# Kernel tuning notes

Measured on AMD Instinct MI355X. Metric: run time of the kernel, lower is better.

The kernel has to match this reference:

```python
import jax, jax.numpy as jnp
import numpy as np

B, N, IN_DIM, HID, OUT, HEADS = 2, 1024, 64, 64, 64, 4
PHD1, PHD2 = HID // HEADS, OUT // HEADS
SLOPE = 0.2  # PyG GATv2Conv default negative_slope
EPS = 1e-12  # F.normalize eps


def _gatv2_dense(x, Wl, Wr, att, bias, heads, phd, mask):
    """Dense GATv2 layer over a full adjacency mask.
    x: [B,N,Din]; Wl/Wr: [Din, heads*phd]; att: [heads,phd]; bias: [heads*phd];
    mask: [N,N] bool, mask[i,j]=True means edge j->i exists.
    """
    Bb, Nn, _ = x.shape
    xl = (x @ Wl).reshape(Bb, Nn, heads, phd)  # source features
    xr = (x @ Wr).reshape(Bb, Nn, heads, phd)  # target features
    # s[b,i,j,h,p] = leaky_relu(xr[b,i] + xl[b,j])  (GATv2)
    s = jax.nn.leaky_relu(xr[:, :, None] + xl[:, None, :], SLOPE)
    e = jnp.einsum('bijhp,hp->bijh', s, att)  # [B,Ni,Nj,H]
    e = jnp.where(mask[None, :, :, None], e, -jnp.inf)
    alpha = jax.nn.softmax(e, axis=2)  # softmax over source nodes j
    out = jnp.einsum('bijh,bjhp->bihp', alpha, xl).reshape(Bb, Nn, heads * phd)
    return out + bias


def setup_inputs() -> dict:
    key = jax.random.key(0)
    ks = jax.random.split(key, 10)
    sc = 0.1
    return {
        'x': jax.random.normal(ks[0], (B, N, IN_DIM), jnp.float32),
        'embedding': jax.random.normal(ks[1], (N, HID), jnp.float32),
        'Wl1': jax.random.normal(ks[2], (IN_DIM, HEADS * PHD1), jnp.float32) * sc,
        'Wr1': jax.random.normal(ks[3], (IN_DIM, HEADS * PHD1), jnp.float32) * sc,
        'att1': jax.random.normal(ks[4], (HEADS, PHD1), jnp.float32) * sc,
        'b1': jnp.zeros((HEADS * PHD1,), jnp.float32),
        'Wl2': jax.random.normal(ks[5], (HID, HEADS * PHD2), jnp.float32) * sc,
        'Wr2': jax.random.normal(ks[6], (HID, HEADS * PHD2), jnp.float32) * sc,
        'att2': jax.random.normal(ks[7], (HEADS, PHD2), jnp.float32) * sc,
        'b2': jnp.zeros((HEADS * PHD2,), jnp.float32),
    }


def reference(x, embedding, Wl1, Wr1, att1, b1, Wl2, Wr2, att2, b2):
    # AdaptiveAdjacency: cosine-similarity adjacency; only its nonzero pattern is used.
    norm = jnp.maximum(jnp.linalg.norm(embedding, axis=1, keepdims=True), EPS)
    ne = embedding / norm
    adj = ne @ ne.T  # [N,N]
    # edge set = adj.nonzero(); GATv2Conv(add_self_loops=True) guarantees diagonal
    mask = (adj != 0) | jnp.eye(N, dtype=bool)
    h = jax.nn.relu(_gatv2_dense(x, Wl1, Wr1, att1, b1, HEADS, PHD1, mask))
    # dropout(0.3) in eval mode -> identity
    return _gatv2_dense(h, Wl2, Wr2, att2, b2, HEADS, PHD2, mask)
```

## Files before the change

kernel.cpp:

```cpp
#include <hip/hip_runtime.h>
#include <math.h>

#define NN 1024
#define BB 2
#define D 64
#define NHEAD 4
#define PH 16
#define LOG2E 1.4426950408889634f

template <int CTRL>
__device__ __forceinline__ float dpp_mov(float x) {
    int xi = __builtin_bit_cast(int, x);
    int r = __builtin_amdgcn_update_dpp(0, xi, CTRL, 0xF, 0xF, true);
    return __builtin_bit_cast(float, r);
}

__device__ __forceinline__ float dpp_rowsum16(float t) {
    t += dpp_mov<0x111>(t);
    t += dpp_mov<0x112>(t);
    t += dpp_mov<0x114>(t);
    t += dpp_mov<0x118>(t);
    return t;
}

__device__ __forceinline__ float quad_sum4(float t) {
    t += dpp_mov<0xB1>(t);
    t += dpp_mov<0x4E>(t);
    return t;
}

#define MST 65
__global__ __launch_bounds__(256) void k_mask(const float* __restrict__ emb,
                                              unsigned char* __restrict__ mask) {
    __shared__ float As[64 * MST];
    __shared__ float Bs[64 * MST];
    int tid = threadIdx.x;
    int ib = (blockIdx.x & 15) << 6;
    int jb = (blockIdx.x >> 4) << 6;

    #pragma unroll
    for (int r = 0; r < 4; ++r) {
        int q = tid + (r << 8);
        int row = q >> 4, c4 = (q & 15) << 2;
        float4 a = *(const float4*)&emb[(ib + row) * D + c4];
        float4 b = *(const float4*)&emb[(jb + row) * D + c4];
        As[row * MST + c4 + 0] = a.x; As[row * MST + c4 + 1] = a.y;
        As[row * MST + c4 + 2] = a.z; As[row * MST + c4 + 3] = a.w;
        Bs[row * MST + c4 + 0] = b.x; Bs[row * MST + c4 + 1] = b.y;
        Bs[row * MST + c4 + 2] = b.z; Bs[row * MST + c4 + 3] = b.w;
    }
    __syncthreads();

    int i0 = (tid >> 4) << 2;
    int j0 = (tid & 15) << 2;
    float acc[4][4] = {};
    #pragma unroll 8
    for (int k = 0; k < 64; ++k) {
        float a0 = As[(i0 + 0) * MST + k];
        float a1 = As[(i0 + 1) * MST + k];
        float a2 = As[(i0 + 2) * MST + k];
        float a3 = As[(i0 + 3) * MST + k];
        float b0 = Bs[(j0 + 0) * MST + k];
        float b1 = Bs[(j0 + 1) * MST + k];
        float b2 = Bs[(j0 + 2) * MST + k];
        float b3 = Bs[(j0 + 3) * MST + k];
        acc[0][0] = fmaf(a0, b0, acc[0][0]); acc[0][1] = fmaf(a0, b1, acc[0][1]);
        acc[0][2] = fmaf(a0, b2, acc[0][2]); acc[0][3] = fmaf(a0, b3, acc[0][3]);
        acc[1][0] = fmaf(a1, b0, acc[1][0]); acc[1][1] = fmaf(a1, b1, acc[1][1]);
        acc[1][2] = fmaf(a1, b2, acc[1][2]); acc[1][3] = fmaf(a1, b3, acc[1][3]);
        acc[2][0] = fmaf(a2, b0, acc[2][0]); acc[2][1] = fmaf(a2, b1, acc[2][1]);
        acc[2][2] = fmaf(a2, b2, acc[2][2]); acc[2][3] = fmaf(a2, b3, acc[2][3]);
        acc[3][0] = fmaf(a3, b0, acc[3][0]); acc[3][1] = fmaf(a3, b1, acc[3][1]);
        acc[3][2] = fmaf(a3, b2, acc[3][2]); acc[3][3] = fmaf(a3, b3, acc[3][3]);
    }
    #pragma unroll
    for (int r = 0; r < 4; ++r) {
        int gi = ib + i0 + r;
        uchar4 m;
        m.x = (acc[r][0] != 0.f || gi == jb + j0 + 0) ? 1 : 0;
        m.y = (acc[r][1] != 0.f || gi == jb + j0 + 1) ? 1 : 0;
        m.z = (acc[r][2] != 0.f || gi == jb + j0 + 2) ? 1 : 0;
        m.w = (acc[r][3] != 0.f || gi == jb + j0 + 3) ? 1 : 0;
        *(uchar4*)&mask[gi * NN + jb + j0] = m;
    }
}

__global__ __launch_bounds__(256) void k_gemm2(const float* __restrict__ A,
                                               const float* __restrict__ Wl,
                                               const float* __restrict__ Wr,
                                               const float* __restrict__ att,
                                               float* __restrict__ xl,
                                               float* __restrict__ xr,
                                               float* __restrict__ alE) {
    __shared__ float wl[64 * 64];
    __shared__ float wr[64 * 64];
    int tid = threadIdx.x;
    for (int t = tid; t < 4096; t += 256) { wl[t] = Wl[t]; wr[t] = Wr[t]; }
    __syncthreads();
    int r = blockIdx.x * 4 + (tid >> 6);
    int c = tid & 63;
    float av = att[c];
    const float* arow = A + r * 64;
    float accl = 0.f, accr = 0.f;
    #pragma unroll
    for (int p = 0; p < 64; ++p) {
        float a = arow[p];
        accl = fmaf(a, wl[p * 64 + c], accl);
        accr = fmaf(a, wr[p * 64 + c], accr);
    }
    xl[r * 64 + c] = accl;
    xr[r * 64 + c] = accr;
    float t = dpp_rowsum16(accl * av);
    if ((c & 15) == 15) alE[(r << 2) | (c >> 4)] = 0.6f * LOG2E * t;
}

template <bool RELU>
__global__ __launch_bounds__(256, 2) void k_attn(
    const float* __restrict__ xl, const float* __restrict__ xr,
    const float* __restrict__ att, const float* __restrict__ alE,
    const float* __restrict__ bias, const unsigned char* __restrict__ mask,
    float* __restrict__ out)
{
    __shared__ float Opart[4][4][4][64];
    __shared__ float Lpart[4][4][4][NHEAD];

    int tid = threadIdx.x;
    int wave = tid >> 6, lane = tid & 63;
    int h = lane & 3, jl = lane >> 2;
    int b = blockIdx.x >> 8;
    int i0 = (blockIdx.x & 255) << 2;
    int j0 = (wave << 8) + (jl << 4);

    const float* xlb = xl + (b << 16);

    float at[16], xr0f[16], xr1f[16], xr2f[16], xr3f[16];
    {
        const float* ap = att + (h << 2);
        const float* r0 = xr + (((b << 10) + i0) << 6) + (h << 2);
        const float* r1 = r0 + 64;
        const float* r2 = r0 + 128;
        const float* r3 = r0 + 192;
        #pragma unroll
        for (int q = 0; q < 4; ++q) {
            *(float4*)&at[q << 2]   = *(const float4*)(ap + (q << 4));
            *(float4*)&xr0f[q << 2] = *(const float4*)(r0 + (q << 4));
            *(float4*)&xr1f[q << 2] = *(const float4*)(r1 + (q << 4));
            *(float4*)&xr2f[q << 2] = *(const float4*)(r2 + (q << 4));
            *(float4*)&xr3f[q << 2] = *(const float4*)(r3 + (q << 4));
        }
        #pragma unroll
        for (int p = 0; p < 16; ++p) at[p] *= 0.4f * LOG2E;
    }
    float ar0q[4], ar1q[4], ar2q[4], ar3q[4];
    #pragma unroll
    for (int q = 0; q < 4; ++q) {
        float p0 = 0.f, p1 = 0.f, p2 = 0.f, p3 = 0.f;
        #pragma unroll
        for (int r = 0; r < 4; ++r) {
            float a = at[(q << 2) + r];
            p0 = fmaf(a, xr0f[(q << 2) + r], p0);
            p1 = fmaf(a, xr1f[(q << 2) + r], p1);
            p2 = fmaf(a, xr2f[(q << 2) + r], p2);
            p3 = fmaf(a, xr3f[(q << 2) + r], p3);
        }
        ar0q[q] = 1.5f * quad_sum4(p0);
        ar1q[q] = 1.5f * quad_sum4(p1);
        ar2q[q] = 1.5f * quad_sum4(p2);
        ar3q[q] = 1.5f * quad_sum4(p3);
    }

    unsigned mb0 = 0, mb1 = 0, mb2 = 0, mb3 = 0;
    {
        const unsigned* m0p = (const unsigned*)(mask + (i0 + 0) * NN + j0);
        const unsigned* m1p = (const unsigned*)(mask + (i0 + 1) * NN + j0);
        const unsigned* m2p = (const unsigned*)(mask + (i0 + 2) * NN + j0);
        const unsigned* m3p = (const unsigned*)(mask + (i0 + 3) * NN + j0);
        #pragma unroll
        for (int q = 0; q < 4; ++q) {
            unsigned w0 = m0p[q], w1 = m1p[q], w2 = m2p[q], w3 = m3p[q];
            mb0 |= ((((w0 >> 0) & 1) | ((w0 >> 7) & 2) | ((w0 >> 14) & 4) | ((w0 >> 21) & 8)) << (q << 2));
            mb1 |= ((((w1 >> 0) & 1) | ((w1 >> 7) & 2) | ((w1 >> 14) & 4) | ((w1 >> 21) & 8)) << (q << 2));
            mb2 |= ((((w2 >> 0) & 1) | ((w2 >> 7) & 2) | ((w2 >> 14) & 4) | ((w2 >> 21) & 8)) << (q << 2));
            mb3 |= ((((w3 >> 0) & 1) | ((w3 >> 7) & 2) | ((w3 >> 14) & 4) | ((w3 >> 21) & 8)) << (q << 2));
        }
    }

    float O0[16], O1[16], O2[16], O3[16];
    float l0q[4] = {}, l1q[4] = {}, l2q[4] = {}, l3q[4] = {};
    #pragma unroll
    for (int p = 0; p < 16; ++p) { O0[p] = 0.f; O1[p] = 0.f; O2[p] = 0.f; O3[p] = 0.f; }

    const float* xrow = xlb + (j0 << 6) + (h << 2);
    const float* alp  = alE + (b << 12) + (j0 << 2);

    #pragma unroll 2
    for (int s = 0; s < 16; ++s) {
        const float* rp = xrow + (s << 6);
        float xv[16];
        *(float4*)&xv[0]  = *(const float4*)(rp);
        *(float4*)&xv[4]  = *(const float4*)(rp + 16);
        *(float4*)&xv[8]  = *(const float4*)(rp + 32);
        *(float4*)&xv[12] = *(const float4*)(rp + 48);
        float alr[4];
        *(float4*)alr = *(const float4*)(alp + (s << 2));
        bool m0 = (mb0 >> s) & 1, m1 = (mb1 >> s) & 1;
        bool m2 = (mb2 >> s) & 1, m3 = (mb3 >> s) & 1;

        #pragma unroll
        for (int q = 0; q < 4; ++q) {
            float p0 = 0.f, p1 = 0.f, p2 = 0.f, p3 = 0.f;
            #pragma unroll
            for (int r = 0; r < 4; ++r) {
                float xvv = xv[(q << 2) + r];
                float a = at[(q << 2) + r];
                p0 = fmaf(a, __builtin_fabsf(xr0f[(q << 2) + r] + xvv), p0);
                p1 = fmaf(a, __builtin_fabsf(xr1f[(q << 2) + r] + xvv), p1);
                p2 = fmaf(a, __builtin_fabsf(xr2f[(q << 2) + r] + xvv), p2);
                p3 = fmaf(a, __builtin_fabsf(xr3f[(q << 2) + r] + xvv), p3);
            }
            float e0 = quad_sum4(p0) + (ar0q[q] + alr[q]);
            float e1 = quad_sum4(p1) + (ar1q[q] + alr[q]);
            float e2 = quad_sum4(p2) + (ar2q[q] + alr[q]);
            float e3 = quad_sum4(p3) + (ar3q[q] + alr[q]);
            float pe0 = m0 ? __builtin_amdgcn_exp2f(e0) : 0.f;
            float pe1 = m1 ? __builtin_amdgcn_exp2f(e1) : 0.f;
            float pe2 = m2 ? __builtin_amdgcn_exp2f(e2) : 0.f;
            float pe3 = m3 ? __builtin_amdgcn_exp2f(e3) : 0.f;
            l0q[q] += pe0; l1q[q] += pe1; l2q[q] += pe2; l3q[q] += pe3;
            #pragma unroll
            for (int r = 0; r < 4; ++r) {
                float xvv = xv[(q << 2) + r];
                O0[(q << 2) + r] = fmaf(pe0, xvv, O0[(q << 2) + r]);
                O1[(q << 2) + r] = fmaf(pe1, xvv, O1[(q << 2) + r]);
                O2[(q << 2) + r] = fmaf(pe2, xvv, O2[(q << 2) + r]);
                O3[(q << 2) + r] = fmaf(pe3, xvv, O3[(q << 2) + r]);
            }
        }
    }

    #pragma unroll
    for (int p = 0; p < 16; ++p) {
        O0[p] += dpp_mov<0x114>(O0[p]);  O0[p] += dpp_mov<0x118>(O0[p]);
        O1[p] += dpp_mov<0x114>(O1[p]);  O1[p] += dpp_mov<0x118>(O1[p]);
        O2[p] += dpp_mov<0x114>(O2[p]);  O2[p] += dpp_mov<0x118>(O2[p]);
        O3[p] += dpp_mov<0x114>(O3[p]);  O3[p] += dpp_mov<0x118>(O3[p]);
    }
    #pragma unroll
    for (int q = 0; q < 4; ++q) {
        l0q[q] += dpp_mov<0x114>(l0q[q]);  l0q[q] += dpp_mov<0x118>(l0q[q]);
        l1q[q] += dpp_mov<0x114>(l1q[q]);  l1q[q] += dpp_mov<0x118>(l1q[q]);
        l2q[q] += dpp_mov<0x114>(l2q[q]);  l2q[q] += dpp_mov<0x118>(l2q[q]);
        l3q[q] += dpp_mov<0x114>(l3q[q]);  l3q[q] += dpp_mov<0x118>(l3q[q]);
    }

    if ((lane & 15) >= 12) {
        int k = lane >> 4;
        #pragma unroll
        for (int q = 0; q < 4; ++q) {
            *(float4*)&Opart[0][wave][k][(q << 4) + (h << 2)] = *(const float4*)&O0[q << 2];
            *(float4*)&Opart[1][wave][k][(q << 4) + (h << 2)] = *(const float4*)&O1[q << 2];
            *(float4*)&Opart[2][wave][k][(q << 4) + (h << 2)] = *(const float4*)&O2[q << 2];
            *(float4*)&Opart[3][wave][k][(q << 4) + (h << 2)] = *(const float4*)&O3[q << 2];
        }
        if (h == 0) {
            #pragma unroll
            for (int q = 0; q < 4; ++q) {
                Lpart[0][wave][k][q] = l0q[q];
                Lpart[1][wave][k][q] = l1q[q];
                Lpart[2][wave][k][q] = l2q[q];
                Lpart[3][wave][k][q] = l3q[q];
            }
        }
    }
    __syncthreads();

    {
        int ii = tid >> 6, c = tid & 63;
        float o = 0.f, l = 0.f;
        #pragma unroll
        for (int w = 0; w < 4; ++w)
            #pragma unroll
            for (int k = 0; k < 4; ++k) {
                o += Opart[ii][w][k][c];
                l += Lpart[ii][w][k][c >> 4];
            }
        float res = o / l + bias[c];
        if (RELU) res = fmaxf(res, 0.f);
        out[((b << 10) + i0 + ii) * D + c] = res;
    }
}

extern "C" void kernel_launch(void* const* d_in, const int* in_sizes, int n_in,
                              void* d_out, int out_size, void* d_ws, size_t ws_size,
                              hipStream_t stream) {
    const float* x    = (const float*)d_in[0];
    const float* emb  = (const float*)d_in[1];
    const float* Wl1  = (const float*)d_in[2];
    const float* Wr1  = (const float*)d_in[3];
    const float* att1 = (const float*)d_in[4];
    const float* b1   = (const float*)d_in[5];
    const float* Wl2  = (const float*)d_in[6];
    const float* Wr2  = (const float*)d_in[7];
    const float* att2 = (const float*)d_in[8];
    const float* b2   = (const float*)d_in[9];
    float* out = (float*)d_out;

    unsigned char* mask = (unsigned char*)d_ws;
    float* xl = (float*)(mask + NN * NN);
    float* xr = xl + BB * NN * D;
    float* hbuf = xr + BB * NN * D;
    float* alE = hbuf + BB * NN * D;

    k_mask<<<256, 256, 0, stream>>>(emb, mask);

    k_gemm2<<<BB * NN / 4, 256, 0, stream>>>(x, Wl1, Wr1, att1, xl, xr, alE);
    k_attn<true><<<BB * NN / 4, 256, 0, stream>>>(xl, xr, att1, alE, b1, mask, hbuf);

    k_gemm2<<<BB * NN / 4, 256, 0, stream>>>(hbuf, Wl2, Wr2, att2, xl, xr, alE);
    k_attn<false><<<BB * NN / 4, 256, 0, stream>>>(xl, xr, att2, alE, b2, mask, out);
}
```

Measured before the change: 132.1 us.

## Double-buffer xl tiles and stage alE via async global-to-LDS loads in attention

In the attention kernel, the per-iteration xl row loads move from direct global loads into a per-wave double-buffered LDS staging area filled with global_load_lds. The next iteration's tile is prefetched while the current one is computed, and an explicit vmcnt wait guards each read. The alE logits are copied into LDS once up front, and the mask loads are issued earlier so they overlap. This aims to hide global load latency in the inner loop, at the cost of about 48KB more LDS per block. The last iteration also prefetches one row past the wave's range, which for the final batch and wave reads past the end of xl.

```diff
diff --git a/kernel.cpp b/kernel.cpp
--- a/kernel.cpp
+++ b/kernel.cpp
@@ -27,6 +27,13 @@
     t += dpp_mov<0xB1>(t);
     t += dpp_mov<0x4E>(t);
     return t;
+}
+
+__device__ __forceinline__ void gload_lds16(const float* g, float* l) {
+    __builtin_amdgcn_global_load_lds(
+        (const __attribute__((address_space(1))) unsigned int*)g,
+        (__attribute__((address_space(3))) unsigned int*)l,
+        16, 0, 0);
 }
 
 #define MST 65
@@ -121,6 +128,8 @@
     const float* __restrict__ bias, const unsigned char* __restrict__ mask,
     float* __restrict__ out)
 {
+    __shared__ __align__(16) float XBUF[4][2][1024];
+    __shared__ __align__(16) float ABUF[4][1024];
     __shared__ float Opart[4][4][4][64];
     __shared__ float Lpart[4][4][4][NHEAD];
 
@@ -133,6 +142,7 @@
 
     const float* xlb = xl + (b << 16);
 
+
     float at[16], xr0f[16], xr1f[16], xr2f[16], xr3f[16];
     {
         const float* ap = att + (h << 2);
@@ -151,6 +161,35 @@
         #pragma unroll
         for (int p = 0; p < 16; ++p) at[p] *= 0.4f * LOG2E;
     }
+    unsigned w0q[4], w1q[4], w2q[4], w3q[4];
+    {
+        const unsigned* m0p = (const unsigned*)(mask + (i0 + 0) * NN + j0);
+        const unsigned* m1p = (const unsigned*)(mask + (i0 + 1) * NN + j0);
+        const unsigned* m2p = (const unsigned*)(mask + (i0 + 2) * NN + j0);
+        const unsigned* m3p = (const unsigned*)(mask + (i0 + 3) * NN + j0);
+        #pragma unroll
+        for (int q = 0; q < 4; ++q) { w0q[q] = m0p[q]; w1q[q] = m1p[q]; w2q[q] = m2p[q]; w3q[q] = m3p[q]; }
+    }
+
+    {
+        const float* ga = alE + (b << 12) + (wave << 10);
+        float* da = &ABUF[wave][0];
+        #pragma unroll
+        for (int t = 0; t < 4; ++t) {
+            int u = (t << 6) + lane;
+            int r = ((u & 15) << 4) | (u >> 4);
+            gload_lds16(ga + (r << 2), da + (t << 8));
+        }
+    }
+    {
+        float* d0 = &XBUF[wave][0][0];
+        const float* g0 = xlb + (((wave << 8) + (jl << 4) + 0) << 6) + (h << 2);
+        gload_lds16(g0,      d0);
+        gload_lds16(g0 + 16, d0 + 256);
+        gload_lds16(g0 + 32, d0 + 512);
+        gload_lds16(g0 + 48, d0 + 768);
+    }
+
     float ar0q[4], ar1q[4], ar2q[4], ar3q[4];
     #pragma unroll
     for (int q = 0; q < 4; ++q) {
@@ -168,21 +207,14 @@
         ar2q[q] = 1.5f * quad_sum4(p2);
         ar3q[q] = 1.5f * quad_sum4(p3);
     }
-
     unsigned mb0 = 0, mb1 = 0, mb2 = 0, mb3 = 0;
-    {
-        const unsigned* m0p = (const unsigned*)(mask + (i0 + 0) * NN + j0);
-        const unsigned* m1p = (const unsigned*)(mask + (i0 + 1) * NN + j0);
-        const unsigned* m2p = (const unsigned*)(mask + (i0 + 2) * NN + j0);
-        const unsigned* m3p = (const unsigned*)(mask + (i0 + 3) * NN + j0);
-        #pragma unroll
-        for (int q = 0; q < 4; ++q) {
-            unsigned w0 = m0p[q], w1 = m1p[q], w2 = m2p[q], w3 = m3p[q];
-            mb0 |= ((((w0 >> 0) & 1) | ((w0 >> 7) & 2) | ((w0 >> 14) & 4) | ((w0 >> 21) & 8)) << (q << 2));
-            mb1 |= ((((w1 >> 0) & 1) | ((w1 >> 7) & 2) | ((w1 >> 14) & 4) | ((w1 >> 21) & 8)) << (q << 2));
-            mb2 |= ((((w2 >> 0) & 1) | ((w2 >> 7) & 2) | ((w2 >> 14) & 4) | ((w2 >> 21) & 8)) << (q << 2));
-            mb3 |= ((((w3 >> 0) & 1) | ((w3 >> 7) & 2) | ((w3 >> 14) & 4) | ((w3 >> 21) & 8)) << (q << 2));
-        }
+    #pragma unroll
+    for (int q = 0; q < 4; ++q) {
+        unsigned w0 = w0q[q], w1 = w1q[q], w2 = w2q[q], w3 = w3q[q];
+        mb0 |= ((((w0 >> 0) & 1) | ((w0 >> 7) & 2) | ((w0 >> 14) & 4) | ((w0 >> 21) & 8)) << (q << 2));
+        mb1 |= ((((w1 >> 0) & 1) | ((w1 >> 7) & 2) | ((w1 >> 14) & 4) | ((w1 >> 21) & 8)) << (q << 2));
+        mb2 |= ((((w2 >> 0) & 1) | ((w2 >> 7) & 2) | ((w2 >> 14) & 4) | ((w2 >> 21) & 8)) << (q << 2));
+        mb3 |= ((((w3 >> 0) & 1) | ((w3 >> 7) & 2) | ((w3 >> 14) & 4) | ((w3 >> 21) & 8)) << (q << 2));
     }
 
     float O0[16], O1[16], O2[16], O3[16];
@@ -190,19 +222,27 @@
     #pragma unroll
     for (int p = 0; p < 16; ++p) { O0[p] = 0.f; O1[p] = 0.f; O2[p] = 0.f; O3[p] = 0.f; }
 
-    const float* xrow = xlb + (j0 << 6) + (h << 2);
-    const float* alp  = alE + (b << 12) + (j0 << 2);
-
     #pragma unroll 2
     for (int s = 0; s < 16; ++s) {
-        const float* rp = xrow + (s << 6);
+        {
+            float* dn = &XBUF[wave][(s + 1) & 1][0];
+            const float* gn = xlb + (((wave << 8) + (jl << 4) + (s + 1)) << 6) + (h << 2);
+            gload_lds16(gn,      dn);
+            gload_lds16(gn + 16, dn + 256);
+            gload_lds16(gn + 32, dn + 512);
+            gload_lds16(gn + 48, dn + 768);
+        }
+        asm volatile("s_waitcnt vmcnt(4)" ::: "memory");
+
+        const float* xb = &XBUF[wave][s & 1][0];
         float xv[16];
-        *(float4*)&xv[0]  = *(const float4*)(rp);
-        *(float4*)&xv[4]  = *(const float4*)(rp + 16);
-        *(float4*)&xv[8]  = *(const float4*)(rp + 32);
-        *(float4*)&xv[12] = *(const float4*)(rp + 48);
+        *(float4*)&xv[0]  = *(const float4*)(xb + (lane << 2));
+        *(float4*)&xv[4]  = *(const float4*)(xb + 256 + (lane << 2));
+        *(float4*)&xv[8]  = *(const float4*)(xb + 512 + (lane << 2));
+        *(float4*)&xv[12] = *(const float4*)(xb + 768 + (lane << 2));
         float alr[4];
-        *(float4*)alr = *(const float4*)(alp + (s << 2));
+        *(float4*)alr = *(const float4*)(&ABUF[wave][(s << 6) + (jl << 2)]);
+
         bool m0 = (mb0 >> s) & 1, m1 = (mb1 >> s) & 1;
         bool m2 = (mb2 >> s) & 1, m3 = (mb3 >> s) & 1;
 
```

Measured after the change: 136.3 us. 3.2% more time.

## Permute xl layout so each lane owns a whole head; fuse mask and first GEMM

Applied to the files above, without the earlier changes.

The first GEMM now writes xl in a permuted column order. In the attention kernel each lane reads a full 16-wide head contiguously and computes the logit locally, which drops the quad_sum4 DPP cross-lane reductions and the per-quad running sums. The mask kernel and the first projection GEMM are merged into one launch using a block-index split, removing one kernel launch and letting the two run at the same time. In exchange, xl is stored in a nonstandard layout that every consumer must agree on, and the shared-memory footprint is unified across both branches.

```diff
diff --git a/kernel.cpp b/kernel.cpp
--- a/kernel.cpp
+++ b/kernel.cpp
@@ -5,8 +5,8 @@
 #define BB 2
 #define D 64
 #define NHEAD 4
-#define PH 16
 #define LOG2E 1.4426950408889634f
+#define MST 65
 
 template <int CTRL>
 __device__ __forceinline__ float dpp_mov(float x) {
@@ -23,65 +23,86 @@
     return t;
 }
 
-__device__ __forceinline__ float quad_sum4(float t) {
-    t += dpp_mov<0xB1>(t);
-    t += dpp_mov<0x4E>(t);
-    return t;
-}
-
-#define MST 65
-__global__ __launch_bounds__(256) void k_mask(const float* __restrict__ emb,
-                                              unsigned char* __restrict__ mask) {
-    __shared__ float As[64 * MST];
-    __shared__ float Bs[64 * MST];
+__global__ __launch_bounds__(256) void k_mask_gemm(
+    const float* __restrict__ emb, unsigned char* __restrict__ mask,
+    const float* __restrict__ A, const float* __restrict__ Wl,
+    const float* __restrict__ Wr, const float* __restrict__ att,
+    float* __restrict__ xl, float* __restrict__ xr, float* __restrict__ alE)
+{
+    __shared__ float SH[64 * MST * 2];
     int tid = threadIdx.x;
-    int ib = (blockIdx.x & 15) << 6;
-    int jb = (blockIdx.x >> 4) << 6;
-
-    #pragma unroll
-    for (int r = 0; r < 4; ++r) {
-        int q = tid + (r << 8);
-        int row = q >> 4, c4 = (q & 15) << 2;
-        float4 a = *(const float4*)&emb[(ib + row) * D + c4];
-        float4 b = *(const float4*)&emb[(jb + row) * D + c4];
-        As[row * MST + c4 + 0] = a.x; As[row * MST + c4 + 1] = a.y;
-        As[row * MST + c4 + 2] = a.z; As[row * MST + c4 + 3] = a.w;
-        Bs[row * MST + c4 + 0] = b.x; Bs[row * MST + c4 + 1] = b.y;
-        Bs[row * MST + c4 + 2] = b.z; Bs[row * MST + c4 + 3] = b.w;
-    }
-    __syncthreads();
-
-    int i0 = (tid >> 4) << 2;
-    int j0 = (tid & 15) << 2;
-    float acc[4][4] = {};
-    #pragma unroll 8
-    for (int k = 0; k < 64; ++k) {
-        float a0 = As[(i0 + 0) * MST + k];
-        float a1 = As[(i0 + 1) * MST + k];
-        float a2 = As[(i0 + 2) * MST + k];
-        float a3 = As[(i0 + 3) * MST + k];
-        float b0 = Bs[(j0 + 0) * MST + k];
-        float b1 = Bs[(j0 + 1) * MST + k];
-        float b2 = Bs[(j0 + 2) * MST + k];
-        float b3 = Bs[(j0 + 3) * MST + k];
-        acc[0][0] = fmaf(a0, b0, acc[0][0]); acc[0][1] = fmaf(a0, b1, acc[0][1]);
-        acc[0][2] = fmaf(a0, b2, acc[0][2]); acc[0][3] = fmaf(a0, b3, acc[0][3]);
-        acc[1][0] = fmaf(a1, b0, acc[1][0]); acc[1][1] = fmaf(a1, b1, acc[1][1]);
-        acc[1][2] = fmaf(a1, b2, acc[1][2]); acc[1][3] = fmaf(a1, b3, acc[1][3]);
-        acc[2][0] = fmaf(a2, b0, acc[2][0]); acc[2][1] = fmaf(a2, b1, acc[2][1]);
-        acc[2][2] = fmaf(a2, b2, acc[2][2]); acc[2][3] = fmaf(a2, b3, acc[2][3]);
-        acc[3][0] = fmaf(a3, b0, acc[3][0]); acc[3][1] = fmaf(a3, b1, acc[3][1]);
-        acc[3][2] = fmaf(a3, b2, acc[3][2]); acc[3][3] = fmaf(a3, b3, acc[3][3]);
-    }
-    #pragma unroll
-    for (int r = 0; r < 4; ++r) {
-        int gi = ib + i0 + r;
-        uchar4 m;
-        m.x = (acc[r][0] != 0.f || gi == jb + j0 + 0) ? 1 : 0;
-        m.y = (acc[r][1] != 0.f || gi == jb + j0 + 1) ? 1 : 0;
-        m.z = (acc[r][2] != 0.f || gi == jb + j0 + 2) ? 1 : 0;
-        m.w = (acc[r][3] != 0.f || gi == jb + j0 + 3) ? 1 : 0;
-        *(uchar4*)&mask[gi * NN + jb + j0] = m;
+    if (blockIdx.x < 256) {
+        float* As = SH;
+        float* Bs = SH + 64 * MST;
+        int ib = (blockIdx.x & 15) << 6;
+        int jb = (blockIdx.x >> 4) << 6;
+
+        #pragma unroll
+        for (int r = 0; r < 4; ++r) {
+            int q = tid + (r << 8);
+            int row = q >> 4, c4 = (q & 15) << 2;
+            float4 a = *(const float4*)&emb[(ib + row) * D + c4];
+            float4 b = *(const float4*)&emb[(jb + row) * D + c4];
+            As[row * MST + c4 + 0] = a.x; As[row * MST + c4 + 1] = a.y;
+            As[row * MST + c4 + 2] = a.z; As[row * MST + c4 + 3] = a.w;
+            Bs[row * MST + c4 + 0] = b.x; Bs[row * MST + c4 + 1] = b.y;
+            Bs[row * MST + c4 + 2] = b.z; Bs[row * MST + c4 + 3] = b.w;
+        }
+        __syncthreads();
+
+        int i0 = (tid >> 4) << 2;
+        int j0 = (tid & 15) << 2;
+        float acc[4][4] = {};
+        #pragma unroll 8
+        for (int k = 0; k < 64; ++k) {
+            float a0 = As[(i0 + 0) * MST + k];
+            float a1 = As[(i0 + 1) * MST + k];
+            float a2 = As[(i0 + 2) * MST + k];
+            float a3 = As[(i0 + 3) * MST + k];
+            float b0 = Bs[(j0 + 0) * MST + k];
+            float b1 = Bs[(j0 + 1) * MST + k];
+            float b2 = Bs[(j0 + 2) * MST + k];
+            float b3 = Bs[(j0 + 3) * MST + k];
+            acc[0][0] = fmaf(a0, b0, acc[0][0]); acc[0][1] = fmaf(a0, b1, acc[0][1]);
+            acc[0][2] = fmaf(a0, b2, acc[0][2]); acc[0][3] = fmaf(a0, b3, acc[0][3]);
+            acc[1][0] = fmaf(a1, b0, acc[1][0]); acc[1][1] = fmaf(a1, b1, acc[1][1]);
+            acc[1][2] = fmaf(a1, b2, acc[1][2]); acc[1][3] = fmaf(a1, b3, acc[1][3]);
+            acc[2][0] = fmaf(a2, b0, acc[2][0]); acc[2][1] = fmaf(a2, b1, acc[2][1]);
+            acc[2][2] = fmaf(a2, b2, acc[2][2]); acc[2][3] = fmaf(a2, b3, acc[2][3]);
+            acc[3][0] = fmaf(a3, b0, acc[3][0]); acc[3][1] = fmaf(a3, b1, acc[3][1]);
+            acc[3][2] = fmaf(a3, b2, acc[3][2]); acc[3][3] = fmaf(a3, b3, acc[3][3]);
+        }
+        #pragma unroll
+        for (int r = 0; r < 4; ++r) {
+            int gi = ib + i0 + r;
+            uchar4 m;
+            m.x = (acc[r][0] != 0.f || gi == jb + j0 + 0) ? 1 : 0;
+            m.y = (acc[r][1] != 0.f || gi == jb + j0 + 1) ? 1 : 0;
+            m.z = (acc[r][2] != 0.f || gi == jb + j0 + 2) ? 1 : 0;
+            m.w = (acc[r][3] != 0.f || gi == jb + j0 + 3) ? 1 : 0;
+            *(uchar4*)&mask[gi * NN + jb + j0] = m;
+        }
+    } else {
+        float* wl = SH;
+        float* wr = SH + 4096;
+        for (int t = tid; t < 4096; t += 256) { wl[t] = Wl[t]; wr[t] = Wr[t]; }
+        __syncthreads();
+        int r = (blockIdx.x - 256) * 4 + (tid >> 6);
+        int c = tid & 63;
+        float av = att[c];
+        const float* arow = A + r * 64;
+        float accl = 0.f, accr = 0.f;
+        #pragma unroll
+        for (int p = 0; p < 64; ++p) {
+            float a = arow[p];
+            accl = fmaf(a, wl[p * 64 + c], accl);
+            accr = fmaf(a, wr[p * 64 + c], accr);
+        }
+        int cp = (((c >> 2) & 3) << 4) | ((c >> 4) << 2) | (c & 3);
+        xl[r * 64 + cp] = accl;
+        xr[r * 64 + c] = accr;
+        float t = dpp_rowsum16(accl * av);
+        if ((c & 15) == 15) alE[(r << 2) | (c >> 4)] = 0.6f * LOG2E * t;
     }
 }
 
@@ -108,7 +129,8 @@
         accl = fmaf(a, wl[p * 64 + c], accl);
         accr = fmaf(a, wr[p * 64 + c], accr);
     }
-    xl[r * 64 + c] = accl;
+    int cp = (((c >> 2) & 3) << 4) | ((c >> 4) << 2) | (c & 3);
+    xl[r * 64 + cp] = accl;
     xr[r * 64 + c] = accr;
     float t = dpp_rowsum16(accl * av);
     if ((c & 15) == 15) alE[(r << 2) | (c >> 4)] = 0.6f * LOG2E * t;
@@ -116,7 +138,7 @@
 
 template <bool RELU>
 __global__ __launch_bounds__(256, 2) void k_attn(
-    const float* __restrict__ xl, const float* __restrict__ xr,
+    const float* __restrict__ xlp, const float* __restrict__ xr,
     const float* __restrict__ att, const float* __restrict__ alE,
     const float* __restrict__ bias, const unsigned char* __restrict__ mask,
     float* __restrict__ out)
@@ -131,42 +153,47 @@
     int i0 = (blockIdx.x & 255) << 2;
     int j0 = (wave << 8) + (jl << 4);
 
-    const float* xlb = xl + (b << 16);
+    const float* xlb = xlp + (b << 16);
 
     float at[16], xr0f[16], xr1f[16], xr2f[16], xr3f[16];
     {
-        const float* ap = att + (h << 2);
-        const float* r0 = xr + (((b << 10) + i0) << 6) + (h << 2);
+        const float* ap = att + (h << 4);
+        const float* r0 = xr + (((b << 10) + i0) << 6) + (h << 4);
         const float* r1 = r0 + 64;
         const float* r2 = r0 + 128;
         const float* r3 = r0 + 192;
         #pragma unroll
-        for (int q = 0; q < 4; ++q) {
-            *(float4*)&at[q << 2]   = *(const float4*)(ap + (q << 4));
-            *(float4*)&xr0f[q << 2] = *(const float4*)(r0 + (q << 4));
-            *(float4*)&xr1f[q << 2] = *(const float4*)(r1 + (q << 4));
-            *(float4*)&xr2f[q << 2] = *(const float4*)(r2 + (q << 4));
-            *(float4*)&xr3f[q << 2] = *(const float4*)(r3 + (q << 4));
+        for (int c = 0; c < 4; ++c) {
+            *(float4*)&at[c << 2]   = *(const float4*)(ap + (c << 2));
+            *(float4*)&xr0f[c << 2] = *(const float4*)(r0 + (c << 2));
+            *(float4*)&xr1f[c << 2] = *(const float4*)(r1 + (c << 2));
+            *(float4*)&xr2f[c << 2] = *(const float4*)(r2 + (c << 2));
+            *(float4*)&xr3f[c << 2] = *(const float4*)(r3 + (c << 2));
         }
         #pragma unroll
         for (int p = 0; p < 16; ++p) at[p] *= 0.4f * LOG2E;
     }
-    float ar0q[4], ar1q[4], ar2q[4], ar3q[4];
-    #pragma unroll
-    for (int q = 0; q < 4; ++q) {
-        float p0 = 0.f, p1 = 0.f, p2 = 0.f, p3 = 0.f;
-        #pragma unroll
-        for (int r = 0; r < 4; ++r) {
-            float a = at[(q << 2) + r];
-            p0 = fmaf(a, xr0f[(q << 2) + r], p0);
-            p1 = fmaf(a, xr1f[(q << 2) + r], p1);
-            p2 = fmaf(a, xr2f[(q << 2) + r], p2);
-            p3 = fmaf(a, xr3f[(q << 2) + r], p3);
-        }
-        ar0q[q] = 1.5f * quad_sum4(p0);
-        ar1q[q] = 1.5f * quad_sum4(p1);
-        ar2q[q] = 1.5f * quad_sum4(p2);
-        ar3q[q] = 1.5f * quad_sum4(p3);
+    float ar0, ar1, ar2, ar3;
+    {
+        float s0[4], s1[4], s2[4], s3[4];
+        #pragma unroll
+        for (int c = 0; c < 4; ++c) {
+            float t0 = 0.f, t1 = 0.f, t2 = 0.f, t3 = 0.f;
+            #pragma unroll
+            for (int r = 0; r < 4; ++r) {
+                int p = (c << 2) + r;
+                float a = at[p];
+                t0 = fmaf(a, xr0f[p], t0);
+                t1 = fmaf(a, xr1f[p], t1);
+                t2 = fmaf(a, xr2f[p], t2);
+                t3 = fmaf(a, xr3f[p], t3);
+            }
+            s0[c] = t0; s1[c] = t1; s2[c] = t2; s3[c] = t3;
+        }
+        ar0 = 1.5f * ((s0[0] + s0[1]) + (s0[2] + s0[3]));
+        ar1 = 1.5f * ((s1[0] + s1[1]) + (s1[2] + s1[3]));
+        ar2 = 1.5f * ((s2[0] + s2[1]) + (s2[2] + s2[3]));
+        ar3 = 1.5f * ((s3[0] + s3[1]) + (s3[2] + s3[3]));
     }
 
     unsigned mb0 = 0, mb1 = 0, mb2 = 0, mb3 = 0;
@@ -186,12 +213,12 @@
     }
 
     float O0[16], O1[16], O2[16], O3[16];
-    float l0q[4] = {}, l1q[4] = {}, l2q[4] = {}, l3q[4] = {};
+    float lq0 = 0.f, lq1 = 0.f, lq2 = 0.f, lq3 = 0.f;
     #pragma unroll
     for (int p = 0; p < 16; ++p) { O0[p] = 0.f; O1[p] = 0.f; O2[p] = 0.f; O3[p] = 0.f; }
 
     const float* xrow = xlb + (j0 << 6) + (h << 2);
-    const float* alp  = alE + (b << 12) + (j0 << 2);
+    const float* alp  = alE + (b << 12) + (j0 << 2) + h;
 
     #pragma unroll 2
     for (int s = 0; s < 16; ++s) {
@@ -201,40 +228,41 @@
         *(float4*)&xv[4]  = *(const float4*)(rp + 16);
         *(float4*)&xv[8]  = *(const float4*)(rp + 32);
         *(float4*)&xv[12] = *(const float4*)(rp + 48);
-        float alr[4];
-        *(float4*)alr = *(const float4*)(alp + (s << 2));
+        float alr = alp[s << 2];
         bool m0 = (mb0 >> s) & 1, m1 = (mb1 >> s) & 1;
         bool m2 = (mb2 >> s) & 1, m3 = (mb3 >> s) & 1;
 
-        #pragma unroll
-        for (int q = 0; q < 4; ++q) {
-            float p0 = 0.f, p1 = 0.f, p2 = 0.f, p3 = 0.f;
+        float s0[4], s1[4], s2[4], s3[4];
+        #pragma unroll
+        for (int c = 0; c < 4; ++c) {
+            float t0 = 0.f, t1 = 0.f, t2 = 0.f, t3 = 0.f;
             #pragma unroll
             for (int r = 0; r < 4; ++r) {
-                float xvv = xv[(q << 2) + r];
-                float a = at[(q << 2) + r];
-                p0 = fmaf(a, __builtin_fabsf(xr0f[(q << 2) + r] + xvv), p0);
-                p1 = fmaf(a, __builtin_fabsf(xr1f[(q << 2) + r] + xvv), p1);
-                p2 = fmaf(a, __builtin_fabsf(xr2f[(q << 2) + r] + xvv), p2);
-                p3 = fmaf(a, __builtin_fabsf(xr3f[(q << 2) + r] + xvv), p3);
+                int p = (c << 2) + r;
+                float a = at[p], xvv = xv[p];
+                t0 = fmaf(a, __builtin_fabsf(xr0f[p] + xvv), t0);
+                t1 = fmaf(a, __builtin_fabsf(xr1f[p] + xvv), t1);
+                t2 = fmaf(a, __builtin_fabsf(xr2f[p] + xvv), t2);
+                t3 = fmaf(a, __builtin_fabsf(xr3f[p] + xvv), t3);
             }
-            float e0 = quad_sum4(p0) + (ar0q[q] + alr[q]);
-            float e1 = quad_sum4(p1) + (ar1q[q] + alr[q]);
-            float e2 = quad_sum4(p2) + (ar2q[q] + alr[q]);
-            float e3 = quad_sum4(p3) + (ar3q[q] + alr[q]);
-            float pe0 = m0 ? __builtin_amdgcn_exp2f(e0) : 0.f;
-            float pe1 = m1 ? __builtin_amdgcn_exp2f(e1) : 0.f;
-            float pe2 = m2 ? __builtin_amdgcn_exp2f(e2) : 0.f;
-            float pe3 = m3 ? __builtin_amdgcn_exp2f(e3) : 0.f;
-            l0q[q] += pe0; l1q[q] += pe1; l2q[q] += pe2; l3q[q] += pe3;
-            #pragma unroll
-            for (int r = 0; r < 4; ++r) {
-                float xvv = xv[(q << 2) + r];
-                O0[(q << 2) + r] = fmaf(pe0, xvv, O0[(q << 2) + r]);
-                O1[(q << 2) + r] = fmaf(pe1, xvv, O1[(q << 2) + r]);
-                O2[(q << 2) + r] = fmaf(pe2, xvv, O2[(q << 2) + r]);
-                O3[(q << 2) + r] = fmaf(pe3, xvv, O3[(q << 2) + r]);
-            }
+            s0[c] = t0; s1[c] = t1; s2[c] = t2; s3[c] = t3;
+        }
+        float e0 = ((s0[0] + s0[1]) + (s0[2] + s0[3])) + (ar0 + alr);
+        float e1 = ((s1[0] + s1[1]) + (s1[2] + s1[3])) + (ar1 + alr);
+        float e2 = ((s2[0] + s2[1]) + (s2[2] + s2[3])) + (ar2 + alr);
+        float e3 = ((s3[0] + s3[1]) + (s3[2] + s3[3])) + (ar3 + alr);
+        float pe0 = m0 ? __builtin_amdgcn_exp2f(e0) : 0.f;
+        float pe1 = m1 ? __builtin_amdgcn_exp2f(e1) : 0.f;
+        float pe2 = m2 ? __builtin_amdgcn_exp2f(e2) : 0.f;
+        float pe3 = m3 ? __builtin_amdgcn_exp2f(e3) : 0.f;
+        lq0 += pe0; lq1 += pe1; lq2 += pe2; lq3 += pe3;
+        #pragma unroll
+        for (int p = 0; p < 16; ++p) {
+            float xvv = xv[p];
+            O0[p] = fmaf(pe0, xvv, O0[p]);
+            O1[p] = fmaf(pe1, xvv, O1[p]);
+            O2[p] = fmaf(pe2, xvv, O2[p]);
+            O3[p] = fmaf(pe3, xvv, O3[p]);
         }
     }
 
@@ -245,32 +273,24 @@
         O2[p] += dpp_mov<0x114>(O2[p]);  O2[p] += dpp_mov<0x118>(O2[p]);
         O3[p] += dpp_mov<0x114>(O3[p]);  O3[p] += dpp_mov<0x118>(O3[p]);
     }
-    #pragma unroll
-    for (int q = 0; q < 4; ++q) {
-        l0q[q] += dpp_mov<0x114>(l0q[q]);  l0q[q] += dpp_mov<0x118>(l0q[q]);
-        l1q[q] += dpp_mov<0x114>(l1q[q]);  l1q[q] += dpp_mov<0x118>(l1q[q]);
-        l2q[q] += dpp_mov<0x114>(l2q[q]);  l2q[q] += dpp_mov<0x118>(l2q[q]);
-        l3q[q] += dpp_mov<0x114>(l3q[q]);  l3q[q] += dpp_mov<0x118>(l3q[q]);
-    }
+    lq0 += dpp_mov<0x114>(lq0);  lq0 += dpp_mov<0x118>(lq0);
+    lq1 += dpp_mov<0x114>(lq1);  lq1 += dpp_mov<0x118>(lq1);
+    lq2 += dpp_mov<0x114>(lq2);  lq2 += dpp_mov<0x118>(lq2);
+    lq3 += dpp_mov<0x114>(lq3);  lq3 += dpp_mov<0x118>(lq3);
 
     if ((lane & 15) >= 12) {
         int k = lane >> 4;
         #pragma unroll
-        for (int q = 0; q < 4; ++q) {
-            *(float4*)&Opart[0][wave][k][(q << 4) + (h << 2)] = *(const float4*)&O0[q << 2];
-            *(float4*)&Opart[1][wave][k][(q << 4) + (h << 2)] = *(const float4*)&O1[q << 2];
-            *(float4*)&Opart[2][wave][k][(q << 4) + (h << 2)] = *(const float4*)&O2[q << 2];
-            *(float4*)&Opart[3][wave][k][(q << 4) + (h << 2)] = *(const float4*)&O3[q << 2];
-        }
-        if (h == 0) {
-            #pragma unroll
-            for (int q = 0; q < 4; ++q) {
-                Lpart[0][wave][k][q] = l0q[q];
-                Lpart[1][wave][k][q] = l1q[q];
-                Lpart[2][wave][k][q] = l2q[q];
-                Lpart[3][wave][k][q] = l3q[q];
-            }
-        }
+        for (int c = 0; c < 4; ++c) {
+            *(float4*)&Opart[0][wave][k][(h << 4) + (c << 2)] = *(const float4*)&O0[c << 2];
+            *(float4*)&Opart[1][wave][k][(h << 4) + (c << 2)] = *(const float4*)&O1[c << 2];
+            *(float4*)&Opart[2][wave][k][(h << 4) + (c << 2)] = *(const float4*)&O2[c << 2];
+            *(float4*)&Opart[3][wave][k][(h << 4) + (c << 2)] = *(const float4*)&O3[c << 2];
+        }
+        Lpart[0][wave][k][h] = lq0;
+        Lpart[1][wave][k][h] = lq1;
+        Lpart[2][wave][k][h] = lq2;
+        Lpart[3][wave][k][h] = lq3;
     }
     __syncthreads();
 
@@ -311,9 +331,7 @@
     float* hbuf = xr + BB * NN * D;
     float* alE = hbuf + BB * NN * D;
 
-    k_mask<<<256, 256, 0, stream>>>(emb, mask);
-
-    k_gemm2<<<BB * NN / 4, 256, 0, stream>>>(x, Wl1, Wr1, att1, xl, xr, alE);
+    k_mask_gemm<<<256 + BB * NN / 4, 256, 0, stream>>>(emb, mask, x, Wl1, Wr1, att1, xl, xr, alE);
     k_attn<true><<<BB * NN / 4, 256, 0, stream>>>(xl, xr, att1, alE, b1, mask, hbuf);
 
     k_gemm2<<<BB * NN / 4, 256, 0, stream>>>(hbuf, Wl2, Wr2, att2, xl, xr, alE);
```

New measurement: 130.4 us. No clear change (-1.3%).
